# Performance work log

Hardware: AMD Instinct MI355X
Metric: run time of the kernel (lower is better)

## Reference

```python
import jax, jax.numpy as jnp
import numpy as np

N_NODES = 50000
N_EDGES = 500000
LN_EPS = 1e-5
COS_EPS = 1e-8


def _layernorm(x, g, b):
    # LayerNorm over last dim, affine
    mu = jnp.mean(x, axis=-1, keepdims=True)
    var = jnp.mean((x - mu) ** 2, axis=-1, keepdims=True)
    return (x - mu) * jax.lax.rsqrt(var + LN_EPS) * g + b


def _filter_conv(x, W, g, b, Bw, Bb, src, dst, heads, ch, concat):
    """One FilterGraphConv layer (eval mode, aggr='add').
    src/dst: raw edge_index rows (no self loops)."""
    N = x.shape[0]
    E = src.shape[0]
    # mu_neb = matmul(adj_t, x, reduce='mean'); adj row=src, col=dst
    deg = jax.ops.segment_sum(jnp.ones((E,), x.dtype), src, num_segments=N)
    mu = jax.ops.segment_sum(x[dst], src, num_segments=N) / jnp.maximum(deg, 1.0)[:, None]
    # x_l = lin_l(x).view(N, H, C); layernorm per head-channel block
    xl = (x @ W).reshape(N, heads, ch)
    xl_ln = _layernorm(xl, g, b)
    # add self loops (inputs guaranteed self-loop-free)
    loop = jnp.arange(N, dtype=src.dtype)
    s2 = jnp.concatenate([src, loop])
    d2 = jnp.concatenate([dst, loop])
    # cosine-similarity attention on neighborhood means
    a = mu[s2]
    c = mu[d2]
    denom = jnp.maximum(jnp.linalg.norm(a, axis=-1) * jnp.linalg.norm(c, axis=-1), COS_EPS)
    alpha = jnp.sum(a * c, axis=-1) / denom  # [E+N]
    # message = LN(x_j) * alpha, scatter-add to destination
    msg = xl_ln[s2] * alpha[:, None, None]  # [E+N, H, C]
    out = jax.ops.segment_sum(msg, d2, num_segments=N)  # [N, H, C]
    out = out.reshape(N, heads * ch) if concat else out.mean(axis=1)
    # bias linear applied to the layer input
    return out + x @ Bw + Bb


def setup_inputs() -> dict:
    key = jax.random.key(0)
    ks = jax.random.split(key, 16)
    N, E = N_NODES, N_EDGES
    x = jax.random.normal(ks[0], (N, 128), jnp.float32)
    src = jax.random.randint(ks[1], (E,), 0, N, dtype=jnp.int32)
    off = jax.random.randint(ks[2], (E,), 1, N, dtype=jnp.int32)
    dst = (src + off) % N  # guaranteed no self loops
    edge_index = jnp.stack([src, dst])

    def glorot(k, shape):
        lim = np.sqrt(6.0 / (shape[0] + shape[1]))
        return jax.random.uniform(k, shape, jnp.float32, -lim, lim)

    return {
        'x': x, 'edge_index': edge_index,
        'W0': glorot(ks[3], (128, 256)), 'g0': jnp.ones((64,)), 'b0': jnp.zeros((64,)),
        'B0': glorot(ks[4], (128, 256)) * 0.1, 'bb0': jax.random.normal(ks[5], (256,)) * 0.01,
        'W1': glorot(ks[6], (256, 256)), 'g1': jnp.ones((64,)), 'b1': jnp.zeros((64,)),
        'B1': glorot(ks[7], (256, 256)) * 0.1, 'bb1': jax.random.normal(ks[8], (256,)) * 0.01,
        'W2': glorot(ks[9], (256, 40)), 'g2': jnp.ones((40,)), 'b2': jnp.zeros((40,)),
        'B2': glorot(ks[10], (256, 1)) * 0.1, 'bb2': jax.random.normal(ks[11], (1,)) * 0.01,
    }


def reference(x, edge_index, W0, g0, b0, B0, bb0, W1, g1, b1, B1, bb1, W2, g2, b2, B2, bb2):
    src, dst = edge_index[0], edge_index[1]
    h = _filter_conv(x, W0, g0, b0, B0, bb0, src, dst, heads=4, ch=64, concat=True)
    h = jax.nn.elu(h)
    h = _filter_conv(h, W1, g1, b1, B1, bb1, src, dst, heads=4, ch=64, concat=True)
    h = jax.nn.elu(h)
    out = _filter_conv(h, W2, g2, b2, B2, bb2, src, dst, heads=1, ch=40, concat=False)
    return jax.nn.log_softmax(out, axis=-1)
```

## Files before the change

kernel.cpp:

```cpp
#include <hip/hip_runtime.h>
#include <math.h>

#define LN_EPS 1e-5f
#define COS_EPS 1e-8f

typedef short bf16x8 __attribute__((ext_vector_type(8)));
typedef float f32x4 __attribute__((ext_vector_type(4)));

static __device__ __forceinline__ unsigned short f2bf(float f) {
    unsigned u = __float_as_uint(f);
    u = u + 0x7FFFu + ((u >> 16) & 1u);
    return (unsigned short)(u >> 16);
}
static __device__ __forceinline__ float bf2f(short s) {
    return __uint_as_float(((unsigned)(unsigned short)s) << 16);
}

template<int EPL>
static __device__ __forceinline__ void loadrow(const short* __restrict__ p, float* r) {
    if constexpr (EPL == 4) {
        short4 v = *reinterpret_cast<const short4*>(p);
        r[0] = bf2f(v.x); r[1] = bf2f(v.y); r[2] = bf2f(v.z); r[3] = bf2f(v.w);
    } else {
        short2 v = *reinterpret_cast<const short2*>(p);
        r[0] = bf2f(v.x); r[1] = bf2f(v.y);
    }
}
template<int EPL>
static __device__ __forceinline__ void storerow(short* __restrict__ p, const float* m) {
    if constexpr (EPL == 4) {
        short4 v;
        v.x = (short)f2bf(m[0]); v.y = (short)f2bf(m[1]);
        v.z = (short)f2bf(m[2]); v.w = (short)f2bf(m[3]);
        *reinterpret_cast<short4*>(p) = v;
    } else {
        short2 v;
        v.x = (short)f2bf(m[0]); v.y = (short)f2bf(m[1]);
        *reinterpret_cast<short2*>(p) = v;
    }
}

__global__ void count_deg(const int* __restrict__ src, const int* __restrict__ dst,
                          int* __restrict__ deg_src, int* __restrict__ deg_dst, int E) {
    int e = blockIdx.x * blockDim.x + threadIdx.x;
    if (e < E) {
        atomicAdd(&deg_src[src[e]], 1);
        atomicAdd(&deg_dst[dst[e]], 1);
    }
}

__global__ void scan_phase1(const int* __restrict__ degA, const int* __restrict__ degB,
                            int* __restrict__ rpA, int* __restrict__ rpB,
                            int* __restrict__ bsA, int* __restrict__ bsB, int n, int nb) {
    __shared__ int sdata[256];
    int bid = blockIdx.x;
    const int* deg; int* rp; int* bs; int seg;
    if (bid < nb) { deg = degA; rp = rpA; bs = bsA; seg = bid; }
    else          { deg = degB; rp = rpB; bs = bsB; seg = bid - nb; }
    int i = seg * 256 + threadIdx.x;
    int v = (i < n) ? deg[i] : 0;
    sdata[threadIdx.x] = v;
    __syncthreads();
    for (int off = 1; off < 256; off <<= 1) {
        int t = (threadIdx.x >= off) ? sdata[threadIdx.x - off] : 0;
        __syncthreads();
        sdata[threadIdx.x] += t;
        __syncthreads();
    }
    if (i < n) rp[i] = sdata[threadIdx.x] - v;
    if (threadIdx.x == 255) bs[seg] = sdata[255];
}

__global__ void scan_phase2(int* __restrict__ bsA, int* __restrict__ bsB, int nb,
                            int* __restrict__ rpA, int* __restrict__ rpB, int n) {
    __shared__ int sdata[256];
    __shared__ int s_carry;
    for (int arr = 0; arr < 2; ++arr) {
        int* bs = arr ? bsB : bsA;
        int* rp = arr ? rpB : rpA;
        if (threadIdx.x == 0) s_carry = 0;
        __syncthreads();
        for (int base = 0; base < nb; base += 256) {
            int i = base + threadIdx.x;
            int v = (i < nb) ? bs[i] : 0;
            sdata[threadIdx.x] = v;
            __syncthreads();
            for (int off = 1; off < 256; off <<= 1) {
                int t = (threadIdx.x >= off) ? sdata[threadIdx.x - off] : 0;
                __syncthreads();
                sdata[threadIdx.x] += t;
                __syncthreads();
            }
            if (i < nb) bs[i] = s_carry + sdata[threadIdx.x] - v;
            __syncthreads();
            if (threadIdx.x == 255) s_carry += sdata[255];
            __syncthreads();
        }
        if (threadIdx.x == 0) rp[n] = s_carry;
        __syncthreads();
    }
}

__global__ void scan_phase3(int* __restrict__ rpA, int* __restrict__ rpB,
                            const int* __restrict__ bsA, const int* __restrict__ bsB,
                            int* __restrict__ curA, int* __restrict__ curB, int n, int nb) {
    int bid = blockIdx.x;
    if (bid < nb) {
        int i = bid * 256 + threadIdx.x;
        if (i < n) { int v = rpA[i] + bsA[bid]; rpA[i] = v; curA[i] = v; }
    } else {
        int seg = bid - nb;
        int i = seg * 256 + threadIdx.x;
        if (i < n) { int v = rpB[i] + bsB[seg]; rpB[i] = v; curB[i] = v; }
    }
}

__global__ void fill_csr(const int* __restrict__ src, const int* __restrict__ dst,
                         int* __restrict__ cur_src, int* __restrict__ cur_dst,
                         long long* __restrict__ CSRS, int* __restrict__ SRCd, int E) {
    int e = blockIdx.x * blockDim.x + threadIdx.x;
    if (e < E) {
        int s = src[e], d = dst[e];
        int p = atomicAdd(&cur_src[s], 1);
        int q = atomicAdd(&cur_dst[d], 1);
        long long packed = (((long long)q) << 32) | (unsigned)d;
        __builtin_nontemporal_store(packed, CSRS + p);
        __builtin_nontemporal_store(s, SRCd + q);
    }
}

__global__ void cast_bf16(const float* __restrict__ X, short* __restrict__ Y, int n4) {
    int i = blockIdx.x * blockDim.x + threadIdx.x;
    if (i >= n4) return;
    float4 v = reinterpret_cast<const float4*>(X)[i];
    short4 o;
    o.x = (short)f2bf(v.x); o.y = (short)f2bf(v.y);
    o.z = (short)f2bf(v.z); o.w = (short)f2bf(v.w);
    reinterpret_cast<short4*>(Y)[i] = o;
}

__global__ void pack_w(const float* __restrict__ W, short* __restrict__ Wp,
                       int KT, int NCT_total, int ct_base, int nct_local, int ncols) {
    int idx = blockIdx.x * blockDim.x + threadIdx.x;
    int total = KT * nct_local * 512;
    if (idx >= total) return;
    int j = idx & 7;
    int l = (idx >> 3) & 63;
    int t = idx >> 9;
    int ctl = t % nct_local;
    int kt = t / nct_local;
    int k = kt * 32 + (l >> 4) * 8 + j;
    int col = ctl * 16 + (l & 15);
    float v = (col < ncols) ? W[(size_t)k * ncols + col] : 0.f;
    Wp[(((size_t)kt * NCT_total + ct_base + ctl) * 64 + l) * 8 + j] = (short)f2bf(v);
}

template<int KT, int NCT, int NCT_A, bool LNF>
__global__ __launch_bounds__(512) void mfma_gemm_v4(const short* __restrict__ Xb,
                                                    const short* __restrict__ Wp,
                                                    short* __restrict__ XL,
                                                    short* __restrict__ XBb,
                                                    const float* __restrict__ g,
                                                    const float* __restrict__ b,
                                                    int M, int CoA) {
    __shared__ short bsm[NCT * 512];
    const int K = KT * 32;
    int lane = threadIdx.x & 63;
    int wave = threadIdx.x >> 6;
    size_t row0 = ((size_t)blockIdx.x * 8 + wave) * 16;
    bool active = row0 < (size_t)M;
    const short* arow = Xb + (row0 + (lane & 15)) * K + (lane >> 4) * 8;

    f32x4 acc[NCT];
#pragma unroll
    for (int ct = 0; ct < NCT; ++ct) {
        f32x4 z = {0.f, 0.f, 0.f, 0.f};
        acc[ct] = z;
    }

#pragma unroll 1
    for (int kt = 0; kt < KT; ++kt) {
        __syncthreads();
        const int4* wsrc = reinterpret_cast<const int4*>(Wp + (size_t)kt * NCT * 512);
        int4* wdst = reinterpret_cast<int4*>(bsm);
        for (int i = threadIdx.x; i < NCT * 64; i += 512) wdst[i] = wsrc[i];
        __syncthreads();
        if (active) {
            bf16x8 a = *reinterpret_cast<const bf16x8*>(arow + kt * 32);
#pragma unroll
            for (int ct = 0; ct < NCT; ++ct) {
                bf16x8 bv = *reinterpret_cast<const bf16x8*>(bsm + ct * 512 + lane * 8);
                acc[ct] = __builtin_amdgcn_mfma_f32_16x16x32_bf16(a, bv, acc[ct], 0, 0, 0);
            }
        }
    }
    if (!active) return;

    int c0 = lane & 15;
    int r0 = (lane >> 4) * 4;
    if constexpr (LNF) {
        float gg[4], bv[4];
#pragma unroll
        for (int m = 0; m < 4; ++m) {
            gg[m] = g[m * 16 + c0];
            bv[m] = b[m * 16 + c0];
        }
#pragma unroll
        for (int h = 0; h < NCT_A / 4; ++h) {
#pragma unroll
            for (int j = 0; j < 4; ++j) {
                float s = acc[4*h+0][j] + acc[4*h+1][j] + acc[4*h+2][j] + acc[4*h+3][j];
                s += __shfl_xor(s, 1, 64); s += __shfl_xor(s, 2, 64);
                s += __shfl_xor(s, 4, 64); s += __shfl_xor(s, 8, 64);
                float mu_ = s * 0.015625f;
                float d0 = acc[4*h+0][j] - mu_, d1 = acc[4*h+1][j] - mu_;
                float d2 = acc[4*h+2][j] - mu_, d3 = acc[4*h+3][j] - mu_;
                float s2 = d0*d0 + d1*d1 + d2*d2 + d3*d3;
                s2 += __shfl_xor(s2, 1, 64); s2 += __shfl_xor(s2, 2, 64);
                s2 += __shfl_xor(s2, 4, 64); s2 += __shfl_xor(s2, 8, 64);
                float rs = rsqrtf(s2 * 0.015625f + LN_EPS);
                size_t row = row0 + r0 + j;
                short* rowp = XL + row * 256 + c0;
                rowp[(4*h+0)*16] = (short)f2bf(d0 * rs * gg[0] + bv[0]);
                rowp[(4*h+1)*16] = (short)f2bf(d1 * rs * gg[1] + bv[1]);
                rowp[(4*h+2)*16] = (short)f2bf(d2 * rs * gg[2] + bv[2]);
                rowp[(4*h+3)*16] = (short)f2bf(d3 * rs * gg[3] + bv[3]);
            }
        }
#pragma unroll
        for (int ct = NCT_A; ct < NCT; ++ct) {
#pragma unroll
            for (int j = 0; j < 4; ++j) {
                size_t row = row0 + r0 + j;
                XBb[row * 256 + (ct - NCT_A) * 16 + c0] = (short)f2bf(acc[ct][j]);
            }
        }
    } else {
#pragma unroll
        for (int ct = 0; ct < NCT; ++ct) {
            int col = ct * 16 + c0;
#pragma unroll
            for (int j = 0; j < 4; ++j) {
                size_t row = row0 + r0 + j;
                if (ct < NCT_A) {
                    if (col < CoA) XL[row * CoA + col] = (short)f2bf(acc[ct][j]);
                } else {
                    XBb[row * 256 + (col - NCT_A * 16)] = (short)f2bf(acc[ct][j]);
                }
            }
        }
    }
}


template<int EPL>
__global__ void mu_norm_v3(const short* __restrict__ Xb, const int* __restrict__ rp,
                           const long long* __restrict__ CSRS, short* __restrict__ MUn,
                           float* __restrict__ NRM, int N) {
    int n = (blockIdx.x * blockDim.x + threadIdx.x) >> 6;
    int lane = threadIdx.x & 63;
    if (n >= N) return;
    const int Fin = EPL * 64;
    int j0 = rp[n], j1 = rp[n + 1];
    float acc[EPL];
#pragma unroll
    for (int k = 0; k < EPL; ++k) acc[k] = 0.f;
    int j = j0;
    for (; j + 8 <= j1; j += 8) {
        int dd[8];
#pragma unroll
        for (int u = 0; u < 8; ++u) dd[u] = (int)CSRS[j + u];
        float r[8][EPL];
#pragma unroll
        for (int u = 0; u < 8; ++u)
            loadrow<EPL>(Xb + (size_t)dd[u] * Fin + lane * EPL, r[u]);
#pragma unroll
        for (int u = 0; u < 8; ++u)
#pragma unroll
            for (int k = 0; k < EPL; ++k) acc[k] += r[u][k];
    }
    for (; j < j1; ++j) {
        int d = (int)CSRS[j];
        float r[EPL];
        loadrow<EPL>(Xb + (size_t)d * Fin + lane * EPL, r);
#pragma unroll
        for (int k = 0; k < EPL; ++k) acc[k] += r[k];
    }
    float inv = 1.f / fmaxf((float)(j1 - j0), 1.f);
    float m[EPL];
    float s = 0.f;
#pragma unroll
    for (int k = 0; k < EPL; ++k) { m[k] = acc[k] * inv; s += m[k] * m[k]; }
    for (int msk = 32; msk > 0; msk >>= 1) s += __shfl_xor(s, msk, 64);
    float nrm = sqrtf(s);
    float innv = 1.f / fmaxf(nrm, 1e-8f);
#pragma unroll
    for (int k = 0; k < EPL; ++k) m[k] *= innv;
    storerow<EPL>(MUn + (size_t)n * Fin + lane * EPL, m);
    if (lane == 0) NRM[n] = nrm;
}

template<int EPL>
__global__ void alpha_v3(const short* __restrict__ MUn, const long long* __restrict__ CSRS,
                         const int* __restrict__ rp_src, float* __restrict__ ALPHAd, int N) {
    int sn = (blockIdx.x * blockDim.x + threadIdx.x) >> 6;
    int lane = threadIdx.x & 63;
    if (sn >= N) return;
    const int Fin = EPL * 64;
    float a[EPL];
    loadrow<EPL>(MUn + (size_t)sn * Fin + lane * EPL, a);
    int j0 = rp_src[sn], j1 = rp_src[sn + 1];
    int j = j0;
    for (; j + 8 <= j1; j += 8) {
        int dd[8], qq[8];
#pragma unroll
        for (int u = 0; u < 8; ++u) {
            long long c = CSRS[j + u];
            dd[u] = (int)c;
            qq[u] = (int)(c >> 32);
        }
        float cr[8][EPL];
#pragma unroll
        for (int u = 0; u < 8; ++u)
            loadrow<EPL>(MUn + (size_t)dd[u] * Fin + lane * EPL, cr[u]);
        float t[8];
#pragma unroll
        for (int u = 0; u < 8; ++u) {
            float tt = 0.f;
#pragma unroll
            for (int k = 0; k < EPL; ++k) tt += a[k] * cr[u][k];
            t[u] = tt;
        }
#pragma unroll
        for (int u = 0; u < 8; ++u)
            for (int msk = 32; msk > 0; msk >>= 1) t[u] += __shfl_xor(t[u], msk, 64);
        if (lane == 0) {
#pragma unroll
            for (int u = 0; u < 8; ++u)
                __builtin_nontemporal_store(t[u], ALPHAd + qq[u]);
        }
    }
    for (; j < j1; ++j) {
        long long c = CSRS[j];
        int d = (int)c, q = (int)(c >> 32);
        float cr[EPL];
        loadrow<EPL>(MUn + (size_t)d * Fin + lane * EPL, cr);
        float t = 0.f;
#pragma unroll
        for (int k = 0; k < EPL; ++k) t += a[k] * cr[k];
        for (int msk = 32; msk > 0; msk >>= 1) t += __shfl_xor(t, msk, 64);
        if (lane == 0) __builtin_nontemporal_store(t, ALPHAd + q);
    }
}

__global__ void ln_kernel_bf(short* __restrict__ XL, const float* __restrict__ g,
                             const float* __restrict__ b, int H, int C) {
    int n = blockIdx.x;
    int h = threadIdx.x >> 6;
    int lane = threadIdx.x & 63;
    size_t idx = (size_t)n * H * C + (size_t)h * C + lane;
    float v = (lane < C) ? bf2f(XL[idx]) : 0.f;
    float s = v;
    for (int msk = 32; msk > 0; msk >>= 1) s += __shfl_xor(s, msk, 64);
    float mu_ = s / (float)C;
    float d = (lane < C) ? (v - mu_) : 0.f;
    float s2 = d * d;
    for (int msk = 32; msk > 0; msk >>= 1) s2 += __shfl_xor(s2, msk, 64);
    float var = s2 / (float)C;
    if (lane < C) {
        float y = (v - mu_) * rsqrtf(var + LN_EPS) * g[lane] + b[lane];
        XL[idx] = (short)f2bf(y);
    }
}

__global__ void scatter_elu_v3(const short* __restrict__ XLN, const float* __restrict__ ALPHAd,
                               const int* __restrict__ rp_dst, const int* __restrict__ SRCd,
                               const float* __restrict__ NRM,
                               const short* __restrict__ XB, const float* __restrict__ bb,
                               short* __restrict__ Yb, int N) {
    int n = (blockIdx.x * blockDim.x + threadIdx.x) >> 6;
    int lane = threadIdx.x & 63;
    if (n >= N) return;
    int j0 = rp_dst[n], j1 = rp_dst[n + 1];
    float acc[4] = {0.f, 0.f, 0.f, 0.f};
    int j = j0;
    for (; j + 8 <= j1; j += 8) {
        int ss[8];
        float aa[8];
#pragma unroll
        for (int u = 0; u < 8; ++u) { ss[u] = SRCd[j + u]; aa[u] = ALPHAd[j + u]; }
        float r[8][4];
#pragma unroll
        for (int u = 0; u < 8; ++u)
            loadrow<4>(XLN + (size_t)ss[u] * 256 + lane * 4, r[u]);
#pragma unroll
        for (int u = 0; u < 8; ++u)
#pragma unroll
            for (int k = 0; k < 4; ++k) acc[k] += r[u][k] * aa[u];
    }
    for (; j < j1; ++j) {
        int s = SRCd[j];
        float a = ALPHAd[j];
        float r[4];
        loadrow<4>(XLN + (size_t)s * 256 + lane * 4, r);
#pragma unroll
        for (int k = 0; k < 4; ++k) acc[k] += r[k] * a;
    }
    float nn = NRM[n], n2 = nn * nn;
    float aself = n2 / fmaxf(n2, COS_EPS);
    float rs[4];
    loadrow<4>(XLN + (size_t)n * 256 + lane * 4, rs);
#pragma unroll
    for (int k = 0; k < 4; ++k) acc[k] += rs[k] * aself;

    float xb[4], o[4];
    loadrow<4>(XB + (size_t)n * 256 + lane * 4, xb);
    float4 bv = *reinterpret_cast<const float4*>(bb + lane * 4);
    o[0] = acc[0] + xb[0] + bv.x; o[1] = acc[1] + xb[1] + bv.y;
    o[2] = acc[2] + xb[2] + bv.z; o[3] = acc[3] + xb[3] + bv.w;
#pragma unroll
    for (int k = 0; k < 4; ++k) o[k] = (o[k] > 0.f) ? o[k] : expm1f(o[k]);
    storerow<4>(Yb + (size_t)n * 256 + lane * 4, o);
}

__global__ void scatter_final_ls(const short* __restrict__ XLN, const float* __restrict__ ALPHAd,
                                 const int* __restrict__ rp_dst, const int* __restrict__ SRCd,
                                 const float* __restrict__ NRM, float* __restrict__ OUT, int N) {
    int n = (blockIdx.x * blockDim.x + threadIdx.x) >> 6;
    int lane = threadIdx.x & 63;
    if (n >= N) return;
    bool act = lane < 40;
    int j0 = rp_dst[n], j1 = rp_dst[n + 1];
    float acc = 0.f;
    int j = j0;
    for (; j + 8 <= j1; j += 8) {
        int ss[8];
        float aa[8];
#pragma unroll
        for (int u = 0; u < 8; ++u) { ss[u] = SRCd[j + u]; aa[u] = ALPHAd[j + u]; }
        float r[8];
#pragma unroll
        for (int u = 0; u < 8; ++u)
            r[u] = act ? bf2f(XLN[(size_t)ss[u] * 40 + lane]) : 0.f;
#pragma unroll
        for (int u = 0; u < 8; ++u) acc += r[u] * aa[u];
    }
    for (; j < j1; ++j) {
        int s = SRCd[j];
        float a = ALPHAd[j];
        float r = act ? bf2f(XLN[(size_t)s * 40 + lane]) : 0.f;
        acc += r * a;
    }
    float nn = NRM[n], n2 = nn * nn;
    float aself = n2 / fmaxf(n2, COS_EPS);
    acc += (act ? bf2f(XLN[(size_t)n * 40 + lane]) : 0.f) * aself;

    float v = act ? acc : -INFINITY;
    float mx = v;
    for (int msk = 32; msk > 0; msk >>= 1) mx = fmaxf(mx, __shfl_xor(mx, msk, 64));
    float ex = act ? expf(v - mx) : 0.f;
    float se = ex;
    for (int msk = 32; msk > 0; msk >>= 1) se += __shfl_xor(se, msk, 64);
    if (act) OUT[(size_t)n * 40 + lane] = v - mx - logf(se);
}

extern "C" void kernel_launch(void* const* d_in, const int* in_sizes, int n_in,
                              void* d_out, int out_size, void* d_ws, size_t ws_size,
                              hipStream_t stream) {
    const float* x   = (const float*)d_in[0];
    const int*   ei  = (const int*)d_in[1];
    const float* W0  = (const float*)d_in[2];
    const float* g0  = (const float*)d_in[3];
    const float* b0  = (const float*)d_in[4];
    const float* B0  = (const float*)d_in[5];
    const float* bb0 = (const float*)d_in[6];
    const float* W1  = (const float*)d_in[7];
    const float* g1  = (const float*)d_in[8];
    const float* b1  = (const float*)d_in[9];
    const float* B1  = (const float*)d_in[10];
    const float* bb1 = (const float*)d_in[11];
    const float* W2  = (const float*)d_in[12];
    const float* g2  = (const float*)d_in[13];
    const float* b2  = (const float*)d_in[14];
    float* out = (float*)d_out;

    const int N = in_sizes[0] / 128;
    const int E = in_sizes[1] / 2;
    const int* src = ei;
    const int* dst = ei + E;

    char* ws = (char*)d_ws;
    size_t off = 0;
    auto alloc = [&](size_t bytes) -> void* {
        void* p = ws + off;
        off += (bytes + 255) & ~(size_t)255;
        return p;
    };
    int* deg_src     = (int*)alloc((size_t)N * 4);
    int* deg_dst     = (int*)alloc((size_t)N * 4);
    int* rp_src      = (int*)alloc((size_t)(N + 1) * 4);
    int* rp_dst      = (int*)alloc((size_t)(N + 1) * 4);
    int* cur_src     = (int*)alloc((size_t)N * 4);
    int* cur_dst     = (int*)alloc((size_t)N * 4);
    int* bs_src      = (int*)alloc((size_t)1024 * 4);
    int* bs_dst      = (int*)alloc((size_t)1024 * 4);
    long long* CSRS  = (long long*)alloc((size_t)E * 8);
    int* SRCd        = (int*)alloc((size_t)E * 4);
    float* ALPHAd    = (float*)alloc((size_t)E * 4);
    float* NRM       = (float*)alloc((size_t)N * 4);
    short* XBb       = (short*)alloc((size_t)N * 256 * 2);
    short* MUn       = (short*)alloc((size_t)N * 256 * 2);
    short* XLb       = (short*)alloc((size_t)N * 256 * 2);
    short* Xb_a      = (short*)alloc((size_t)N * 256 * 2);
    short* Xb_b      = (short*)alloc((size_t)N * 256 * 2);
    short* Wp        = (short*)alloc((size_t)8 * 32 * 64 * 8 * 2);
    (void)ws_size;

    hipMemsetAsync(deg_src, 0, (size_t)N * 4, stream);
    hipMemsetAsync(deg_dst, 0, (size_t)N * 4, stream);
    int egrid = (E + 255) / 256;
    count_deg<<<egrid, 256, 0, stream>>>(src, dst, deg_src, deg_dst, E);
    int nb = (N + 255) / 256;
    scan_phase1<<<2 * nb, 256, 0, stream>>>(deg_src, deg_dst, rp_src, rp_dst,
                                            bs_src, bs_dst, N, nb);
    scan_phase2<<<1, 256, 0, stream>>>(bs_src, bs_dst, nb, rp_src, rp_dst, N);
    scan_phase3<<<2 * nb, 256, 0, stream>>>(rp_src, rp_dst, bs_src, bs_dst,
                                            cur_src, cur_dst, N, nb);
    fill_csr<<<egrid, 256, 0, stream>>>(src, dst, cur_src, cur_dst, CSRS, SRCd, E);

    {
        int n4 = (N * 128) / 4;
        cast_bf16<<<(n4 + 255) / 256, 256, 0, stream>>>(x, Xb_a, n4);
    }

    int wgridN = (N * 64 + 255) / 256;
    int ggrid  = (N + 127) / 128;

    mu_norm_v3<2><<<wgridN, 256, 0, stream>>>(Xb_a, rp_src, CSRS, MUn, NRM, N);
    alpha_v3<2><<<wgridN, 256, 0, stream>>>(MUn, CSRS, rp_src, ALPHAd, N);
    {
        int tot = 4 * 16 * 512;
        pack_w<<<(tot + 255) / 256, 256, 0, stream>>>(W0, Wp, 4, 32, 0, 16, 256);
        pack_w<<<(tot + 255) / 256, 256, 0, stream>>>(B0, Wp, 4, 32, 16, 16, 256);
    }
    mfma_gemm_v4<4, 32, 16, true><<<ggrid, 512, 0, stream>>>(Xb_a, Wp, XLb, XBb,
                                                             g0, b0, N, 256);
    scatter_elu_v3<<<wgridN, 256, 0, stream>>>(XLb, ALPHAd, rp_dst, SRCd, NRM,
                                               XBb, bb0, Xb_b, N);

    mu_norm_v3<4><<<wgridN, 256, 0, stream>>>(Xb_b, rp_src, CSRS, MUn, NRM, N);
    alpha_v3<4><<<wgridN, 256, 0, stream>>>(MUn, CSRS, rp_src, ALPHAd, N);
    {
        int tot = 8 * 16 * 512;
        pack_w<<<(tot + 255) / 256, 256, 0, stream>>>(W1, Wp, 8, 32, 0, 16, 256);
        pack_w<<<(tot + 255) / 256, 256, 0, stream>>>(B1, Wp, 8, 32, 16, 16, 256);
    }
    mfma_gemm_v4<8, 32, 16, true><<<ggrid, 512, 0, stream>>>(Xb_b, Wp, XLb, XBb,
                                                             g1, b1, N, 256);
    scatter_elu_v3<<<wgridN, 256, 0, stream>>>(XLb, ALPHAd, rp_dst, SRCd, NRM,
                                               XBb, bb1, Xb_a, N);

    mu_norm_v3<4><<<wgridN, 256, 0, stream>>>(Xb_a, rp_src, CSRS, MUn, NRM, N);
    alpha_v3<4><<<wgridN, 256, 0, stream>>>(MUn, CSRS, rp_src, ALPHAd, N);
    {
        int tot = 8 * 3 * 512;
        pack_w<<<(tot + 255) / 256, 256, 0, stream>>>(W2, Wp, 8, 3, 0, 3, 40);
    }
    mfma_gemm_v4<8, 3, 3, false><<<ggrid, 512, 0, stream>>>(Xb_a, Wp, XLb, nullptr,
                                                            nullptr, nullptr, N, 40);
    ln_kernel_bf<<<N, 64, 0, stream>>>(XLb, g2, b2, 1, 40);
    scatter_final_ls<<<wgridN, 256, 0, stream>>>(XLb, ALPHAd, rp_dst, SRCd, NRM, out, N);
}
```

Before: 764.9 us.

## Fuse cosine attention computation into destination-side scatter kernels

Removes the separate alpha kernel that computed per-edge cosine similarities in source-CSR order and wrote them to a per-edge array. Each scatter kernel now loads the destination node's normalized mean and, for every incoming edge, gathers the source node's normalized mean and computes the dot product inline before weighting the message. The CSR-by-source array shrinks from packed 64-bit to 32-bit since the edge position no longer needs storing. This saves a kernel launch plus the alpha write and read, but adds an extra row gather per edge inside the scatter loop and halves the unroll depth.

```diff
diff --git a/kernel.cpp b/kernel.cpp
--- a/kernel.cpp
+++ b/kernel.cpp
@@ -117,14 +117,13 @@
 
 __global__ void fill_csr(const int* __restrict__ src, const int* __restrict__ dst,
                          int* __restrict__ cur_src, int* __restrict__ cur_dst,
-                         long long* __restrict__ CSRS, int* __restrict__ SRCd, int E) {
+                         int* __restrict__ CSRS, int* __restrict__ SRCd, int E) {
     int e = blockIdx.x * blockDim.x + threadIdx.x;
     if (e < E) {
         int s = src[e], d = dst[e];
         int p = atomicAdd(&cur_src[s], 1);
         int q = atomicAdd(&cur_dst[d], 1);
-        long long packed = (((long long)q) << 32) | (unsigned)d;
-        __builtin_nontemporal_store(packed, CSRS + p);
+        __builtin_nontemporal_store(d, CSRS + p);
         __builtin_nontemporal_store(s, SRCd + q);
     }
 }
@@ -255,7 +254,7 @@
 
 template<int EPL>
 __global__ void mu_norm_v3(const short* __restrict__ Xb, const int* __restrict__ rp,
-                           const long long* __restrict__ CSRS, short* __restrict__ MUn,
+                           const int* __restrict__ CSRS, short* __restrict__ MUn,
                            float* __restrict__ NRM, int N) {
     int n = (blockIdx.x * blockDim.x + threadIdx.x) >> 6;
     int lane = threadIdx.x & 63;
@@ -269,7 +268,7 @@
     for (; j + 8 <= j1; j += 8) {
         int dd[8];
 #pragma unroll
-        for (int u = 0; u < 8; ++u) dd[u] = (int)CSRS[j + u];
+        for (int u = 0; u < 8; ++u) dd[u] = CSRS[j + u];
         float r[8][EPL];
 #pragma unroll
         for (int u = 0; u < 8; ++u)
@@ -280,7 +279,7 @@
             for (int k = 0; k < EPL; ++k) acc[k] += r[u][k];
     }
     for (; j < j1; ++j) {
-        int d = (int)CSRS[j];
+        int d = CSRS[j];
         float r[EPL];
         loadrow<EPL>(Xb + (size_t)d * Fin + lane * EPL, r);
 #pragma unroll
@@ -298,59 +297,6 @@
     for (int k = 0; k < EPL; ++k) m[k] *= innv;
     storerow<EPL>(MUn + (size_t)n * Fin + lane * EPL, m);
     if (lane == 0) NRM[n] = nrm;
-}
-
-template<int EPL>
-__global__ void alpha_v3(const short* __restrict__ MUn, const long long* __restrict__ CSRS,
-                         const int* __restrict__ rp_src, float* __restrict__ ALPHAd, int N) {
-    int sn = (blockIdx.x * blockDim.x + threadIdx.x) >> 6;
-    int lane = threadIdx.x & 63;
-    if (sn >= N) return;
-    const int Fin = EPL * 64;
-    float a[EPL];
-    loadrow<EPL>(MUn + (size_t)sn * Fin + lane * EPL, a);
-    int j0 = rp_src[sn], j1 = rp_src[sn + 1];
-    int j = j0;
-    for (; j + 8 <= j1; j += 8) {
-        int dd[8], qq[8];
-#pragma unroll
-        for (int u = 0; u < 8; ++u) {
-            long long c = CSRS[j + u];
-            dd[u] = (int)c;
-            qq[u] = (int)(c >> 32);
-        }
-        float cr[8][EPL];
-#pragma unroll
-        for (int u = 0; u < 8; ++u)
-            loadrow<EPL>(MUn + (size_t)dd[u] * Fin + lane * EPL, cr[u]);
-        float t[8];
-#pragma unroll
-        for (int u = 0; u < 8; ++u) {
-            float tt = 0.f;
-#pragma unroll
-            for (int k = 0; k < EPL; ++k) tt += a[k] * cr[u][k];
-            t[u] = tt;
-        }
-#pragma unroll
-        for (int u = 0; u < 8; ++u)
-            for (int msk = 32; msk > 0; msk >>= 1) t[u] += __shfl_xor(t[u], msk, 64);
-        if (lane == 0) {
-#pragma unroll
-            for (int u = 0; u < 8; ++u)
-                __builtin_nontemporal_store(t[u], ALPHAd + qq[u]);
-        }
-    }
-    for (; j < j1; ++j) {
-        long long c = CSRS[j];
-        int d = (int)c, q = (int)(c >> 32);
-        float cr[EPL];
-        loadrow<EPL>(MUn + (size_t)d * Fin + lane * EPL, cr);
-        float t = 0.f;
-#pragma unroll
-        for (int k = 0; k < EPL; ++k) t += a[k] * cr[k];
-        for (int msk = 32; msk > 0; msk >>= 1) t += __shfl_xor(t, msk, 64);
-        if (lane == 0) __builtin_nontemporal_store(t, ALPHAd + q);
-    }
 }
 
 __global__ void ln_kernel_bf(short* __restrict__ XL, const float* __restrict__ g,
@@ -373,38 +319,59 @@
     }
 }
 
-__global__ void scatter_elu_v3(const short* __restrict__ XLN, const float* __restrict__ ALPHAd,
-                               const int* __restrict__ rp_dst, const int* __restrict__ SRCd,
-                               const float* __restrict__ NRM,
-                               const short* __restrict__ XB, const float* __restrict__ bb,
-                               short* __restrict__ Yb, int N) {
+template<int EPLM>
+__global__ void scatter_fused_elu(const short* __restrict__ MUn, const short* __restrict__ XLN,
+                                  const int* __restrict__ rp_dst, const int* __restrict__ SRCd,
+                                  const float* __restrict__ NRM,
+                                  const short* __restrict__ XB, const float* __restrict__ bb,
+                                  short* __restrict__ Yb, int N) {
     int n = (blockIdx.x * blockDim.x + threadIdx.x) >> 6;
     int lane = threadIdx.x & 63;
     if (n >= N) return;
+    const int FinM = EPLM * 64;
+    float mn[EPLM];
+    loadrow<EPLM>(MUn + (size_t)n * FinM + lane * EPLM, mn);
     int j0 = rp_dst[n], j1 = rp_dst[n + 1];
     float acc[4] = {0.f, 0.f, 0.f, 0.f};
     int j = j0;
-    for (; j + 8 <= j1; j += 8) {
-        int ss[8];
-        float aa[8];
-#pragma unroll
-        for (int u = 0; u < 8; ++u) { ss[u] = SRCd[j + u]; aa[u] = ALPHAd[j + u]; }
-        float r[8][4];
-#pragma unroll
-        for (int u = 0; u < 8; ++u)
-            loadrow<4>(XLN + (size_t)ss[u] * 256 + lane * 4, r[u]);
-#pragma unroll
-        for (int u = 0; u < 8; ++u)
-#pragma unroll
-            for (int k = 0; k < 4; ++k) acc[k] += r[u][k] * aa[u];
+    for (; j + 4 <= j1; j += 4) {
+        int ss[4];
+#pragma unroll
+        for (int u = 0; u < 4; ++u) ss[u] = SRCd[j + u];
+        float ms[4][EPLM], xl[4][4];
+#pragma unroll
+        for (int u = 0; u < 4; ++u)
+            loadrow<EPLM>(MUn + (size_t)ss[u] * FinM + lane * EPLM, ms[u]);
+#pragma unroll
+        for (int u = 0; u < 4; ++u)
+            loadrow<4>(XLN + (size_t)ss[u] * 256 + lane * 4, xl[u]);
+        float t[4];
+#pragma unroll
+        for (int u = 0; u < 4; ++u) {
+            float tt = 0.f;
+#pragma unroll
+            for (int k = 0; k < EPLM; ++k) tt += mn[k] * ms[u][k];
+            t[u] = tt;
+        }
+#pragma unroll
+        for (int u = 0; u < 4; ++u)
+            for (int msk = 32; msk > 0; msk >>= 1) t[u] += __shfl_xor(t[u], msk, 64);
+#pragma unroll
+        for (int u = 0; u < 4; ++u)
+#pragma unroll
+            for (int k = 0; k < 4; ++k) acc[k] += xl[u][k] * t[u];
     }
     for (; j < j1; ++j) {
         int s = SRCd[j];
-        float a = ALPHAd[j];
-        float r[4];
-        loadrow<4>(XLN + (size_t)s * 256 + lane * 4, r);
-#pragma unroll
-        for (int k = 0; k < 4; ++k) acc[k] += r[k] * a;
+        float ms[EPLM], xl[4];
+        loadrow<EPLM>(MUn + (size_t)s * FinM + lane * EPLM, ms);
+        loadrow<4>(XLN + (size_t)s * 256 + lane * 4, xl);
+        float t = 0.f;
+#pragma unroll
+        for (int k = 0; k < EPLM; ++k) t += mn[k] * ms[k];
+        for (int msk = 32; msk > 0; msk >>= 1) t += __shfl_xor(t, msk, 64);
+#pragma unroll
+        for (int k = 0; k < 4; ++k) acc[k] += xl[k] * t;
     }
     float nn = NRM[n], n2 = nn * nn;
     float aself = n2 / fmaxf(n2, COS_EPS);
@@ -423,33 +390,48 @@
     storerow<4>(Yb + (size_t)n * 256 + lane * 4, o);
 }
 
-__global__ void scatter_final_ls(const short* __restrict__ XLN, const float* __restrict__ ALPHAd,
-                                 const int* __restrict__ rp_dst, const int* __restrict__ SRCd,
-                                 const float* __restrict__ NRM, float* __restrict__ OUT, int N) {
+__global__ void scatter_final_fused(const short* __restrict__ MUn, const short* __restrict__ XLN,
+                                    const int* __restrict__ rp_dst, const int* __restrict__ SRCd,
+                                    const float* __restrict__ NRM, float* __restrict__ OUT,
+                                    int N) {
     int n = (blockIdx.x * blockDim.x + threadIdx.x) >> 6;
     int lane = threadIdx.x & 63;
     if (n >= N) return;
     bool act = lane < 40;
+    float mn[4];
+    loadrow<4>(MUn + (size_t)n * 256 + lane * 4, mn);
     int j0 = rp_dst[n], j1 = rp_dst[n + 1];
     float acc = 0.f;
     int j = j0;
-    for (; j + 8 <= j1; j += 8) {
-        int ss[8];
-        float aa[8];
-#pragma unroll
-        for (int u = 0; u < 8; ++u) { ss[u] = SRCd[j + u]; aa[u] = ALPHAd[j + u]; }
-        float r[8];
-#pragma unroll
-        for (int u = 0; u < 8; ++u)
-            r[u] = act ? bf2f(XLN[(size_t)ss[u] * 40 + lane]) : 0.f;
-#pragma unroll
-        for (int u = 0; u < 8; ++u) acc += r[u] * aa[u];
+    for (; j + 4 <= j1; j += 4) {
+        int ss[4];
+#pragma unroll
+        for (int u = 0; u < 4; ++u) ss[u] = SRCd[j + u];
+        float ms[4][4], xl[4];
+#pragma unroll
+        for (int u = 0; u < 4; ++u)
+            loadrow<4>(MUn + (size_t)ss[u] * 256 + lane * 4, ms[u]);
+#pragma unroll
+        for (int u = 0; u < 4; ++u)
+            xl[u] = act ? bf2f(XLN[(size_t)ss[u] * 40 + lane]) : 0.f;
+        float t[4];
+#pragma unroll
+        for (int u = 0; u < 4; ++u)
+            t[u] = mn[0]*ms[u][0] + mn[1]*ms[u][1] + mn[2]*ms[u][2] + mn[3]*ms[u][3];
+#pragma unroll
+        for (int u = 0; u < 4; ++u)
+            for (int msk = 32; msk > 0; msk >>= 1) t[u] += __shfl_xor(t[u], msk, 64);
+#pragma unroll
+        for (int u = 0; u < 4; ++u) acc += xl[u] * t[u];
     }
     for (; j < j1; ++j) {
         int s = SRCd[j];
-        float a = ALPHAd[j];
-        float r = act ? bf2f(XLN[(size_t)s * 40 + lane]) : 0.f;
-        acc += r * a;
+        float ms[4];
+        loadrow<4>(MUn + (size_t)s * 256 + lane * 4, ms);
+        float xl = act ? bf2f(XLN[(size_t)s * 40 + lane]) : 0.f;
+        float t = mn[0]*ms[0] + mn[1]*ms[1] + mn[2]*ms[2] + mn[3]*ms[3];
+        for (int msk = 32; msk > 0; msk >>= 1) t += __shfl_xor(t, msk, 64);
+        acc += xl * t;
     }
     float nn = NRM[n], n2 = nn * nn;
     float aself = n2 / fmaxf(n2, COS_EPS);
@@ -504,9 +486,8 @@
     int* cur_dst     = (int*)alloc((size_t)N * 4);
     int* bs_src      = (int*)alloc((size_t)1024 * 4);
     int* bs_dst      = (int*)alloc((size_t)1024 * 4);
-    long long* CSRS  = (long long*)alloc((size_t)E * 8);
+    int* CSRS        = (int*)alloc((size_t)E * 4);
     int* SRCd        = (int*)alloc((size_t)E * 4);
-    float* ALPHAd    = (float*)alloc((size_t)E * 4);
     float* NRM       = (float*)alloc((size_t)N * 4);
     short* XBb       = (short*)alloc((size_t)N * 256 * 2);
     short* MUn       = (short*)alloc((size_t)N * 256 * 2);
@@ -537,7 +518,6 @@
     int ggrid  = (N + 127) / 128;
 
     mu_norm_v3<2><<<wgridN, 256, 0, stream>>>(Xb_a, rp_src, CSRS, MUn, NRM, N);
-    alpha_v3<2><<<wgridN, 256, 0, stream>>>(MUn, CSRS, rp_src, ALPHAd, N);
     {
         int tot = 4 * 16 * 512;
         pack_w<<<(tot + 255) / 256, 256, 0, stream>>>(W0, Wp, 4, 32, 0, 16, 256);
@@ -545,11 +525,10 @@
     }
     mfma_gemm_v4<4, 32, 16, true><<<ggrid, 512, 0, stream>>>(Xb_a, Wp, XLb, XBb,
                                                              g0, b0, N, 256);
-    scatter_elu_v3<<<wgridN, 256, 0, stream>>>(XLb, ALPHAd, rp_dst, SRCd, NRM,
-                                               XBb, bb0, Xb_b, N);
+    scatter_fused_elu<2><<<wgridN, 256, 0, stream>>>(MUn, XLb, rp_dst, SRCd, NRM,
+                                                     XBb, bb0, Xb_b, N);
 
     mu_norm_v3<4><<<wgridN, 256, 0, stream>>>(Xb_b, rp_src, CSRS, MUn, NRM, N);
-    alpha_v3<4><<<wgridN, 256, 0, stream>>>(MUn, CSRS, rp_src, ALPHAd, N);
     {
         int tot = 8 * 16 * 512;
         pack_w<<<(tot + 255) / 256, 256, 0, stream>>>(W1, Wp, 8, 32, 0, 16, 256);
@@ -557,11 +536,10 @@
     }
     mfma_gemm_v4<8, 32, 16, true><<<ggrid, 512, 0, stream>>>(Xb_b, Wp, XLb, XBb,
                                                              g1, b1, N, 256);
-    scatter_elu_v3<<<wgridN, 256, 0, stream>>>(XLb, ALPHAd, rp_dst, SRCd, NRM,
-                                               XBb, bb1, Xb_a, N);
+    scatter_fused_elu<4><<<wgridN, 256, 0, stream>>>(MUn, XLb, rp_dst, SRCd, NRM,
+                                                     XBb, bb1, Xb_a, N);
 
     mu_norm_v3<4><<<wgridN, 256, 0, stream>>>(Xb_a, rp_src, CSRS, MUn, NRM, N);
-    alpha_v3<4><<<wgridN, 256, 0, stream>>>(MUn, CSRS, rp_src, ALPHAd, N);
     {
         int tot = 8 * 3 * 512;
         pack_w<<<(tot + 255) / 256, 256, 0, stream>>>(W2, Wp, 8, 3, 0, 3, 40);
@@ -569,5 +547,5 @@
     mfma_gemm_v4<8, 3, 3, false><<<ggrid, 512, 0, stream>>>(Xb_a, Wp, XLb, nullptr,
                                                             nullptr, nullptr, N, 40);
     ln_kernel_bf<<<N, 64, 0, stream>>>(XLb, g2, b2, 1, 40);
-    scatter_final_ls<<<wgridN, 256, 0, stream>>>(XLb, ALPHAd, rp_dst, SRCd, NRM, out, N);
-}
+    scatter_final_fused<<<wgridN, 256, 0, stream>>>(MUn, XLb, rp_dst, SRCd, NRM, out, N);
+}
```

After: 681.7 us. -10.9%, faster.
